# Performance work log

Hardware: AMD Instinct MI355X
Metric: run time of the kernel (lower is better)

Reference implementation:

```python
import jax, jax.numpy as jnp
import numpy as np

ENC_DIM = 1024
NUM_HEADS = 16
HEAD_DIM = ENC_DIM // NUM_HEADS
D_FF = 4 * ENC_DIM
EPS = 1e-5


def _layernorm(x, g, b):
    mu = jnp.mean(x, axis=-1, keepdims=True)
    var = jnp.mean((x - mu) ** 2, axis=-1, keepdims=True)
    return (x - mu) * jax.lax.rsqrt(var + EPS) * g + b


def setup_inputs() -> dict:
    key = jax.random.key(0)
    ks = jax.random.split(key, 12)
    s = 1.0 / np.sqrt(ENC_DIM)
    sf = 1.0 / np.sqrt(D_FF)
    x = jax.random.normal(ks[0], (2, 2048, ENC_DIM), dtype=jnp.float32)
    return {
        "x": x,
        "ln1_g": jnp.ones((ENC_DIM,), jnp.float32),
        "ln1_b": jnp.zeros((ENC_DIM,), jnp.float32),
        "wq": jax.random.uniform(ks[1], (ENC_DIM, ENC_DIM), jnp.float32, -s, s),
        "bq": jax.random.uniform(ks[2], (ENC_DIM,), jnp.float32, -s, s),
        "wk": jax.random.uniform(ks[3], (ENC_DIM, ENC_DIM), jnp.float32, -s, s),
        "bk": jax.random.uniform(ks[4], (ENC_DIM,), jnp.float32, -s, s),
        "wv": jax.random.uniform(ks[5], (ENC_DIM, ENC_DIM), jnp.float32, -s, s),
        "bv": jax.random.uniform(ks[6], (ENC_DIM,), jnp.float32, -s, s),
        "wo": jax.random.uniform(ks[7], (ENC_DIM, ENC_DIM), jnp.float32, -s, s),
        "bo": jax.random.uniform(ks[8], (ENC_DIM,), jnp.float32, -s, s),
        "w1": jax.random.uniform(ks[9], (ENC_DIM, D_FF), jnp.float32, -s, s),
        "b1": jax.random.uniform(ks[10], (D_FF,), jnp.float32, -s, s),
        "w2": jax.random.uniform(ks[11], (D_FF, ENC_DIM), jnp.float32, -sf, sf),
        "b2": jnp.zeros((ENC_DIM,), jnp.float32),
        "ln2_g": jnp.ones((ENC_DIM,), jnp.float32),
        "ln2_b": jnp.zeros((ENC_DIM,), jnp.float32),
    }


def reference(x, ln1_g, ln1_b, wq, bq, wk, bk, wv, bv, wo, bo, w1, b1, w2, b2, ln2_g, ln2_b):
    B, S, D = x.shape
    h = _layernorm(x, ln1_g, ln1_b)
    # QKV projections -> (B, H, S, hd)
    def split_heads(t):
        return t.reshape(B, S, NUM_HEADS, HEAD_DIM).transpose(0, 2, 1, 3)
    q = split_heads(h @ wq + bq)
    k = split_heads(h @ wk + bk)
    v = split_heads(h @ wv + bv)
    scores = jnp.einsum("bhqd,bhkd->bhqk", q, k) / np.sqrt(HEAD_DIM)
    probs = jax.nn.softmax(scores, axis=-1)
    attn = jnp.einsum("bhqk,bhkd->bhqd", probs, v)
    attn = attn.transpose(0, 2, 1, 3).reshape(B, S, D)
    x = attn @ wo + bo + x  # residual 1
    h2 = _layernorm(x, ln2_g, ln2_b)
    mlp = jax.nn.gelu(h2 @ w1 + b1, approximate=False) @ w2 + b2
    return x + mlp
```

## Files before the change

### kernel.cpp

```cpp
#include <hip/hip_runtime.h>

typedef unsigned short u16;
typedef unsigned int u32;
typedef __bf16 bf16x8 __attribute__((ext_vector_type(8)));
typedef float floatx4 __attribute__((ext_vector_type(4)));

__device__ __forceinline__ u16 f2bf(float f) {
    u32 u = __float_as_uint(f);
    u = (u + 0x7FFFu + ((u >> 16) & 1u)) >> 16;
    return (u16)u;
}

__device__ __forceinline__ void gld_lds16(const u16* g, u16* l) {
    __builtin_amdgcn_global_load_lds(
        (const __attribute__((address_space(1))) u32*)g,
        (__attribute__((address_space(3))) u32*)l, 16, 0, 0);
}

__device__ __forceinline__ float gelu_exact(float v) {
    const float z = fabsf(v) * 0.70710678118f;
    const float t = __builtin_amdgcn_rcpf(1.0f + 0.3275911f * z);
    const float e = __builtin_amdgcn_exp2f(-z * z * 1.44269504f);
    float poly = 1.061405429f;
    poly = poly * t - 1.453152027f;
    poly = poly * t + 1.421413741f;
    poly = poly * t - 0.284496736f;
    poly = poly * t + 0.254829592f;
    float erfz = 1.0f - poly * t * e;
    erfz = copysignf(erfz, v);
    return 0.5f * v * (1.0f + erfz);
}

__global__ __launch_bounds__(256) void transpose_cvt4(
    const float* __restrict__ s0, const float* __restrict__ s1,
    const float* __restrict__ s2, const float* __restrict__ s3,
    u16* __restrict__ d0, u16* __restrict__ d1,
    u16* __restrict__ d2, u16* __restrict__ d3)
{
    __shared__ float t[32][33];
    const int z = blockIdx.z;
    const float* src = z == 0 ? s0 : (z == 1 ? s1 : (z == 2 ? s2 : s3));
    u16* dst = z == 0 ? d0 : (z == 1 ? d1 : (z == 2 ? d2 : d3));
    const int bm = blockIdx.x * 32, bk = blockIdx.y * 32;
    const int tx = threadIdx.x & 31, ty = threadIdx.x >> 5;
    #pragma unroll
    for (int i = ty; i < 32; i += 8)
        t[i][tx] = src[(long)(bk + i) * 1024 + bm + tx];
    __syncthreads();
    #pragma unroll
    for (int i = ty; i < 32; i += 8)
        dst[(long)(bm + i) * 1024 + bk + tx] = f2bf(t[tx][i]);
}

__global__ __launch_bounds__(256) void transpose_cvt(
    const float* __restrict__ src, u16* __restrict__ dst, int K, int M)
{
    __shared__ float t[32][33];
    const int bm = blockIdx.x * 32, bk = blockIdx.y * 32;
    const int tx = threadIdx.x & 31, ty = threadIdx.x >> 5;
    #pragma unroll
    for (int i = ty; i < 32; i += 8)
        t[i][tx] = src[(long)(bk + i) * M + bm + tx];
    __syncthreads();
    #pragma unroll
    for (int i = ty; i < 32; i += 8)
        dst[(long)(bm + i) * K + bk + tx] = f2bf(t[tx][i]);
}

__global__ __launch_bounds__(256) void ln_kernel(
    const float* __restrict__ x, const float* __restrict__ g,
    const float* __restrict__ bta, u16* __restrict__ out)
{
    const int row = blockIdx.x;
    const int tid = threadIdx.x;
    const float4 v = ((const float4*)(x + (long)row * 1024))[tid];
    float s  = v.x + v.y + v.z + v.w;
    float s2 = v.x*v.x + v.y*v.y + v.z*v.z + v.w*v.w;
    #pragma unroll
    for (int off = 1; off < 64; off <<= 1) {
        s  += __shfl_xor(s, off);
        s2 += __shfl_xor(s2, off);
    }
    __shared__ float red[8];
    const int wave = tid >> 6, lane = tid & 63;
    if (lane == 0) { red[wave] = s; red[4 + wave] = s2; }
    __syncthreads();
    s  = red[0] + red[1] + red[2] + red[3];
    s2 = red[4] + red[5] + red[6] + red[7];
    const float mu   = s * (1.0f / 1024.0f);
    const float var  = s2 * (1.0f / 1024.0f) - mu * mu;
    const float rstd = rsqrtf(var + 1e-5f);
    const int c = tid << 2;
    ushort4 o;
    o.x = f2bf((v.x - mu) * rstd * g[c + 0] + bta[c + 0]);
    o.y = f2bf((v.y - mu) * rstd * g[c + 1] + bta[c + 1]);
    o.z = f2bf((v.z - mu) * rstd * g[c + 2] + bta[c + 2]);
    o.w = f2bf((v.w - mu) * rstd * g[c + 3] + bta[c + 3]);
    ((ushort4*)(out + (long)row * 1024))[tid] = o;
}

__global__ __launch_bounds__(256) void vtrans_kernel(
    const u16* __restrict__ V, u16* __restrict__ Vt)
{
    __shared__ u16 t[64][72];
    const int bh = blockIdx.y, s0 = blockIdx.x << 6;
    const int tid = threadIdx.x;
    const long base = (long)bh * 2048 * 64;
    const int row = tid >> 2, seg = tid & 3;
    *(uint4*)&t[row][seg << 3] =
        *(const uint4*)(V + base + (long)(s0 + row) * 64 + (seg << 3));
    *(uint4*)&t[row][(seg + 4) << 3] =
        *(const uint4*)(V + base + (long)(s0 + row) * 64 + ((seg + 4) << 3));
    __syncthreads();
    #pragma unroll
    for (int half = 0; half < 2; ++half) {
        const int sl = (seg + (half << 2)) << 3;
        u16 tmp[8];
        #pragma unroll
        for (int j = 0; j < 8; ++j) tmp[j] = t[sl + j][row];
        *(uint4*)(Vt + base + (long)row * 2048 + s0 + sl) = *(uint4*)tmp;
    }
}

template<int MODE>
__global__ __launch_bounds__(512, 2) void gemm256_kernel(
    const u16* __restrict__ A, const u16* __restrict__ Bt,
    const float* __restrict__ bias0, const float* __restrict__ bias1,
    const float* __restrict__ bias2, const float* __restrict__ res,
    float* __restrict__ outf, void* __restrict__ outv, int K, int M)
{
    __shared__ u16 As[2][256 * 64];
    __shared__ u16 Bs[2][256 * 64];
    const int tid = threadIdx.x, lane = tid & 63, wave = tid >> 6;
    const int wr = wave >> 2, wc = wave & 3;
    const int lrow = lane & 15, quad = lane >> 4, sl = lrow & 7;

    const int nwg = gridDim.x * gridDim.y * gridDim.z;
    const int lin = blockIdx.x + gridDim.x * (blockIdx.y + gridDim.y * blockIdx.z);
    const int wg  = (lin & 7) * (nwg >> 3) + (lin >> 3);
    const int bx  = wg % gridDim.x;
    const int rest = wg / gridDim.x;
    const int by  = rest % gridDim.y;
    const int bz  = rest / gridDim.y;

    const long rowbase = (long)by * 256;
    const long colbase = (long)bx * 256;
    int kstart = 0, kend = K;
    if constexpr (MODE == 3) { kstart = bz * (K >> 2); kend = kstart + (K >> 2); }

    const u16* gA[4]; int lA[4];
    const u16* gB[4]; int lB[4];
    #pragma unroll
    for (int i = 0; i < 4; ++i) {
        const int cid = (i << 9) + tid;
        const int rl = cid >> 3, p = cid & 7, q = p ^ (rl & 7);
        gA[i] = A  + (rowbase + rl) * (long)K + kstart + (q << 3);
        gB[i] = Bt + (colbase + rl) * (long)K + kstart + (q << 3);
        lA[i] = rl * 64 + (p << 3);
        lB[i] = rl * 64 + (p << 3);
    }

    floatx4 acc[8][4];
    #pragma unroll
    for (int i = 0; i < 8; ++i)
        #pragma unroll
        for (int j = 0; j < 4; ++j)
            acc[i][j] = floatx4{0.f, 0.f, 0.f, 0.f};

    #pragma unroll
    for (int i = 0; i < 4; ++i) { gld_lds16(gA[i], As[0] + lA[i]); gA[i] += 64; }
    #pragma unroll
    for (int i = 0; i < 4; ++i) { gld_lds16(gB[i], Bs[0] + lB[i]); gB[i] += 64; }
    asm volatile("s_waitcnt vmcnt(0)" ::: "memory");
    __builtin_amdgcn_s_barrier();
    __builtin_amdgcn_sched_barrier(0);

    const int niter = (kend - kstart) >> 6;
    int cur = 0;
    for (int t = 0; t < niter; ++t) {
        if (t + 1 < niter) {
            #pragma unroll
            for (int i = 0; i < 4; ++i) { gld_lds16(gA[i], As[cur ^ 1] + lA[i]); gA[i] += 64; }
            #pragma unroll
            for (int i = 0; i < 4; ++i) { gld_lds16(gB[i], Bs[cur ^ 1] + lB[i]); gB[i] += 64; }
        }

        const u16* as = As[cur];
        const u16* bs = Bs[cur];

        bf16x8 bfr[4][2];
        #pragma unroll
        for (int ns = 0; ns < 4; ++ns)
            #pragma unroll
            for (int kc = 0; kc < 2; ++kc)
                bfr[ns][kc] = *(const bf16x8*)
                    &bs[((wc << 6) + (ns << 4) + lrow) * 64 + ((((kc << 2) + quad) ^ sl) << 3)];

        #pragma unroll
        for (int p = 0; p < 4; ++p) {
            bf16x8 af[2][2];
            #pragma unroll
            for (int m = 0; m < 2; ++m)
                #pragma unroll
                for (int kc = 0; kc < 2; ++kc)
                    af[m][kc] = *(const bf16x8*)
                        &as[((wr << 7) + ((p * 2 + m) << 4) + lrow) * 64 + ((((kc << 2) + quad) ^ sl) << 3)];
            __builtin_amdgcn_s_setprio(1);
            #pragma unroll
            for (int kc = 0; kc < 2; ++kc)
                #pragma unroll
                for (int m = 0; m < 2; ++m)
                    #pragma unroll
                    for (int ns = 0; ns < 4; ++ns)
                        acc[p * 2 + m][ns] = __builtin_amdgcn_mfma_f32_16x16x32_bf16(
                            af[m][kc], bfr[ns][kc], acc[p * 2 + m][ns], 0, 0, 0);
            __builtin_amdgcn_s_setprio(0);
        }

        asm volatile("s_waitcnt lgkmcnt(0)" ::: "memory");
        asm volatile("s_waitcnt vmcnt(0)" ::: "memory");
        __builtin_amdgcn_s_barrier();
        __builtin_amdgcn_sched_barrier(0);
        cur ^= 1;
    }

    #pragma unroll
    for (int ms = 0; ms < 8; ++ms) {
        #pragma unroll
        for (int ns = 0; ns < 4; ++ns) {
            const long col = colbase + (wc << 6) + (ns << 4) + lrow;
            float bv = 0.f;
            if constexpr (MODE == 0) {
                const int which = (int)(col >> 10);
                const float* bp = which == 0 ? bias0 : (which == 1 ? bias1 : bias2);
                bv = bp[col & 1023];
            } else if constexpr (MODE == 2) {
                bv = bias0[col];
            }
            #pragma unroll
            for (int r = 0; r < 4; ++r) {
                const long row = rowbase + (wr << 7) + (ms << 4) + (quad << 2) + r;
                float v = acc[ms][ns][r] + bv;
                if constexpr (MODE == 0) {
                    const long which = col >> 10;
                    if (which == 0) v *= 0.18033688f;
                    const long b = row >> 11, s = row & 2047;
                    const long h = (col >> 6) & 15, d = col & 63;
                    ((u16*)outv)[which * 4194304 + (((b << 4) + h) * 2048 + s) * 64 + d] = f2bf(v);
                } else if constexpr (MODE == 2) {
                    ((u16*)outv)[row * M + col] = f2bf(gelu_exact(v));
                } else {
                    const long idx = row * M + col;
                    if (bz == 0) v += bias0[col] + res[idx];
                    atomicAdd(&outf[idx], v);
                }
            }
        }
    }
}

__global__ __launch_bounds__(256) void gemm_oproj_kernel(
    const u16* __restrict__ A, const u16* __restrict__ Bt,
    const float* __restrict__ bias0, const float* __restrict__ res,
    float* __restrict__ out, int K, int M)
{
    constexpr int MS = 2, NIB = 2;
    __shared__ u16 As[128 * 64];
    __shared__ u16 Bs[64 * 64];
    const int tid = threadIdx.x, lane = tid & 63, wave = tid >> 6;
    const int wm = wave << 5, wn = 0;
    const int lrow = lane & 15, quad = lane >> 4;
    const int sl = lrow & 7;

    const int nwg = gridDim.x * gridDim.y;
    const int lin = blockIdx.x + gridDim.x * blockIdx.y;
    const int wg  = (lin & 7) * (nwg >> 3) + (lin >> 3);
    const int bx  = wg % gridDim.x;
    const int by  = wg / gridDim.x;

    const long rowbase = (long)by * 128;
    const long colbase = (long)bx * 64;

    const u16* gA[4]; int lA[4];
    #pragma unroll
    for (int i = 0; i < 4; ++i) {
        const int cid = (i << 6) + lane;
        const int rl = cid >> 3, p = cid & 7, q = p ^ (rl & 7);
        gA[i] = A + (rowbase + (wave << 5) + rl) * (long)K + (q << 3);
        lA[i] = ((wave << 5) + rl) * 64 + (p << 3);
    }
    const u16* gB[NIB]; int lB[NIB];
    #pragma unroll
    for (int i = 0; i < NIB; ++i) {
        const int cid = (i << 6) + lane;
        const int rl = cid >> 3, p = cid & 7, q = p ^ (rl & 7);
        gB[i] = Bt + (colbase + (wave << 4) + rl) * (long)K + (q << 3);
        lB[i] = ((wave << 4) + rl) * 64 + (p << 3);
    }

    floatx4 acc[MS][4];
    #pragma unroll
    for (int i = 0; i < MS; ++i)
        #pragma unroll
        for (int j = 0; j < 4; ++j)
            acc[i][j] = floatx4{0.f, 0.f, 0.f, 0.f};

    for (int k0 = 0; k0 < K; k0 += 64) {
        __syncthreads();
        #pragma unroll
        for (int i = 0; i < 4; ++i) { gld_lds16(gA[i], As + lA[i]); gA[i] += 64; }
        #pragma unroll
        for (int i = 0; i < NIB; ++i) { gld_lds16(gB[i], Bs + lB[i]); gB[i] += 64; }
        __syncthreads();
        #pragma unroll
        for (int kc = 0; kc < 2; ++kc) {
            const int ph = (((kc << 2) + quad) ^ sl) << 3;
            bf16x8 af[MS], bf[4];
            #pragma unroll
            for (int ms = 0; ms < MS; ++ms)
                af[ms] = *(const bf16x8*)&As[(wm + (ms << 4) + lrow) * 64 + ph];
            #pragma unroll
            for (int ns = 0; ns < 4; ++ns)
                bf[ns] = *(const bf16x8*)&Bs[(wn + (ns << 4) + lrow) * 64 + ph];
            #pragma unroll
            for (int ms = 0; ms < MS; ++ms)
                #pragma unroll
                for (int ns = 0; ns < 4; ++ns)
                    acc[ms][ns] = __builtin_amdgcn_mfma_f32_16x16x32_bf16(
                        af[ms], bf[ns], acc[ms][ns], 0, 0, 0);
        }
    }

    #pragma unroll
    for (int ms = 0; ms < MS; ++ms) {
        #pragma unroll
        for (int ns = 0; ns < 4; ++ns) {
            const long col = colbase + wn + (ns << 4) + lrow;
            const float bv = bias0[col];
            #pragma unroll
            for (int r = 0; r < 4; ++r) {
                const long row = rowbase + wm + (ms << 4) + (quad << 2) + r;
                const long idx = row * M + col;
                out[idx] = acc[ms][ns][r] + bv + res[idx];
            }
        }
    }
}

__global__ __launch_bounds__(512) void attn_kernel(
    const u16* __restrict__ Q, const u16* __restrict__ Kp,
    const u16* __restrict__ Vt, u16* __restrict__ O)
{
    __shared__ u16 Ks[2][4096];
    __shared__ u16 Vs[2][4096];
    __shared__ u16 Ps[8][16][72];
    const int tid = threadIdx.x, lane = tid & 63, wave = tid >> 6;
    const int lrow = lane & 15, quad = lane >> 4;

    const int lin = blockIdx.x;
    const int nl  = ((lin & 7) << 6) + (lin >> 3);
    const int bh  = nl >> 4;
    const int qt  = nl & 15;
    const long kvbase = (long)bh * 2048 * 64;
    const int qbase = (qt << 7) + (wave << 4);

    const int srow = lane >> 3;
    const int schunk = (lane & 7) ^ srow;
    const int c = wave & 3;
    const bool isV = wave >= 4;
    const int lofs = c << 10;
    const u16* g0 = isV
        ? (Vt + kvbase + (long)(((c << 4) + srow) * 2048 + (schunk << 3)))
        : (Kp + kvbase + (long)(((c << 4) + srow) * 64   + (schunk << 3)));
    const u16* g1 = g0 + (isV ? 8 * 2048 : 8 * 64);
    const int gstep = isV ? 64 : 4096;
    u16* lb0 = isV ? &Vs[0][lofs] : &Ks[0][lofs];
    u16* lb1 = isV ? &Vs[1][lofs] : &Ks[1][lofs];

    bf16x8 qf[2];
    #pragma unroll
    for (int h = 0; h < 2; ++h)
        qf[h] = *(const bf16x8*)(Q + kvbase +
            (long)(qbase + lrow) * 64 + (quad << 3) + (h << 5));

    int aoff[4][2];
    #pragma unroll
    for (int ns = 0; ns < 4; ++ns)
        #pragma unroll
        for (int h = 0; h < 2; ++h)
            aoff[ns][h] = ((ns << 4) + lrow) * 64 +
                          (((quad + (h << 2)) ^ (lrow & 7)) << 3);

    floatx4 oacc[4];
    #pragma unroll
    for (int ns = 0; ns < 4; ++ns)
        oacc[ns] = floatx4{0.f, 0.f, 0.f, 0.f};
    float lr = 0.f;

    gld_lds16(g0, lb0);
    gld_lds16(g1, lb0 + 512);
    g0 += gstep; g1 += gstep;

    for (int it = 0; it < 32; ++it) {
        const int cur = it & 1;
        __syncthreads();
        if (it < 31) {
            u16* dst = cur ? lb0 : lb1;
            gld_lds16(g0, dst);
            gld_lds16(g1, dst + 512);
            g0 += gstep; g1 += gstep;
        }
        const u16* ks = &Ks[cur][0];
        const u16* vs = &Vs[cur][0];

        floatx4 st[4];
        __builtin_amdgcn_s_setprio(1);
        #pragma unroll
        for (int ns = 0; ns < 4; ++ns) {
            const bf16x8 af0 = *(const bf16x8*)&ks[aoff[ns][0]];
            const bf16x8 af1 = *(const bf16x8*)&ks[aoff[ns][1]];
            floatx4 z = floatx4{0.f, 0.f, 0.f, 0.f};
            st[ns] = __builtin_amdgcn_mfma_f32_16x16x32_bf16(af0, qf[0], z, 0, 0, 0);
            st[ns] = __builtin_amdgcn_mfma_f32_16x16x32_bf16(af1, qf[1], st[ns], 0, 0, 0);
        }
        __builtin_amdgcn_s_setprio(0);

        float rs = 0.f;
        #pragma unroll
        for (int ns = 0; ns < 4; ++ns) {
            const float p0 = __builtin_amdgcn_exp2f(st[ns][0]);
            const float p1 = __builtin_amdgcn_exp2f(st[ns][1]);
            const float p2 = __builtin_amdgcn_exp2f(st[ns][2]);
            const float p3 = __builtin_amdgcn_exp2f(st[ns][3]);
            rs += (p0 + p1) + (p2 + p3);
            uint2 w;
            w.x = __builtin_amdgcn_perm(__float_as_uint(p1) + 0x8000u,
                                        __float_as_uint(p0) + 0x8000u, 0x07060302u);
            w.y = __builtin_amdgcn_perm(__float_as_uint(p3) + 0x8000u,
                                        __float_as_uint(p2) + 0x8000u, 0x07060302u);
            *(uint2*)&Ps[wave][lrow][(ns << 4) + (quad << 2)] = w;
        }
        rs += __shfl_xor(rs, 16);
        rs += __shfl_xor(rs, 32);
        lr += rs;
        const bf16x8 pf0 = *(const bf16x8*)&Ps[wave][lrow][quad << 3];
        const bf16x8 pf1 = *(const bf16x8*)&Ps[wave][lrow][(quad << 3) + 32];

        __builtin_amdgcn_s_setprio(1);
        #pragma unroll
        for (int ns = 0; ns < 4; ++ns) {
            const bf16x8 vf0 = *(const bf16x8*)&vs[aoff[ns][0]];
            const bf16x8 vf1 = *(const bf16x8*)&vs[aoff[ns][1]];
            oacc[ns] = __builtin_amdgcn_mfma_f32_16x16x32_bf16(pf0, vf0, oacc[ns], 0, 0, 0);
            oacc[ns] = __builtin_amdgcn_mfma_f32_16x16x32_bf16(pf1, vf1, oacc[ns], 0, 0, 0);
        }
        __builtin_amdgcn_s_setprio(0);
    }

    const int b = bh >> 4, h = bh & 15;
    float linv[4];
    #pragma unroll
    for (int r = 0; r < 4; ++r)
        linv[r] = 1.0f / __shfl(lr, (quad << 2) + r);
    #pragma unroll
    for (int ns = 0; ns < 4; ++ns)
        #pragma unroll
        for (int r = 0; r < 4; ++r) {
            const int q = qbase + (quad << 2) + r;
            const long token = (long)b * 2048 + q;
            O[token * 1024 + (h << 6) + (ns << 4) + lrow] =
                f2bf(oacc[ns][r] * linv[r]);
        }
}

extern "C" void kernel_launch(void* const* d_in, const int* in_sizes, int n_in,
                              void* d_out, int out_size, void* d_ws, size_t ws_size,
                              hipStream_t stream)
{
    const float* x     = (const float*)d_in[0];
    const float* ln1_g = (const float*)d_in[1];
    const float* ln1_b = (const float*)d_in[2];
    const float* wq    = (const float*)d_in[3];
    const float* bq    = (const float*)d_in[4];
    const float* wk    = (const float*)d_in[5];
    const float* bk    = (const float*)d_in[6];
    const float* wv    = (const float*)d_in[7];
    const float* bv    = (const float*)d_in[8];
    const float* wo    = (const float*)d_in[9];
    const float* bo    = (const float*)d_in[10];
    const float* w1    = (const float*)d_in[11];
    const float* b1    = (const float*)d_in[12];
    const float* w2    = (const float*)d_in[13];
    const float* b2    = (const float*)d_in[14];
    const float* ln2_g = (const float*)d_in[15];
    const float* ln2_b = (const float*)d_in[16];
    float* out = (float*)d_out;

    char* w = (char*)d_ws;
    const size_t MB = 1024 * 1024;
    u16*   wqkvt = (u16*)(w + 0);
    u16*   wot   = (u16*)(w + 6  * MB);
    u16*   w1t   = (u16*)(w + 8  * MB);
    u16*   w2t   = (u16*)(w + 16 * MB);
    u16*   h1    = (u16*)(w + 24 * MB);
    u16*   qkvb  = (u16*)(w + 32 * MB);
    u16*   vtb   = (u16*)(w + 56 * MB);
    float* x1    = (float*)(w + 64 * MB);
    u16*   ffb   = (u16*)(w + 32 * MB);
    u16*   qb = qkvb;
    u16*   kb = qkvb + 4194304;
    u16*   vb = qkvb + 8388608;

    transpose_cvt4<<<dim3(32, 32, 4), 256, 0, stream>>>(
        wq, wk, wv, wo, wqkvt, wqkvt + 1048576, wqkvt + 2097152, wot);
    transpose_cvt<<<dim3(128, 32), 256, 0, stream>>>(w1, w1t, 1024, 4096);
    transpose_cvt<<<dim3(32, 128), 256, 0, stream>>>(w2, w2t, 4096, 1024);

    ln_kernel<<<4096, 256, 0, stream>>>(x, ln1_g, ln1_b, h1);

    gemm256_kernel<0><<<dim3(12, 16), 512, 0, stream>>>(
        h1, wqkvt, bq, bk, bv, nullptr, nullptr, qkvb, 1024, 3072);

    vtrans_kernel<<<dim3(32, 32), 256, 0, stream>>>(vb, vtb);

    attn_kernel<<<dim3(512), 512, 0, stream>>>(qb, kb, vtb, h1);

    gemm_oproj_kernel<<<dim3(16, 32), 256, 0, stream>>>(
        h1, wot, bo, x, x1, 1024, 1024);

    ln_kernel<<<4096, 256, 0, stream>>>(x1, ln2_g, ln2_b, h1);

    gemm256_kernel<2><<<dim3(16, 16), 512, 0, stream>>>(
        h1, w1t, b1, nullptr, nullptr, nullptr, nullptr, ffb, 1024, 4096);

    hipMemsetAsync(out, 0, (size_t)4096 * 1024 * 4, stream);
    gemm256_kernel<3><<<dim3(4, 16, 4), 512, 0, stream>>>(
        ffb, w2t, b2, nullptr, nullptr, x1, out, nullptr, 4096, 1024);
}
```

Measured before the change: 407.4 us.

## Replace atomic split-K FF2 GEMM with 128-tile 2-way split and add pass

The second MLP GEMM previously used 256x256 tiles with 4-way split-K, a memset of the output and atomicAdd epilogues. It now uses a dedicated 128x128-tile kernel with 2-way split-K. One half writes bias plus residual plus partial sum to the output and the other half writes to a scratch buffer, and a separate elementwise kernel then adds the two. This removes the memset and the atomic traffic, and the smaller tiles give 512 workgroups. In exchange there is an extra kernel launch, an extra full-tensor read/write pass, and less data reuse per tile.

Result: faster. 345.5 us (-15.2%).

```diff
diff --git a/kernel.cpp b/kernel.cpp
--- a/kernel.cpp
+++ b/kernel.cpp
@@ -99,6 +99,20 @@
     ((ushort4*)(out + (long)row * 1024))[tid] = o;
 }
 
+__global__ __launch_bounds__(256) void add_kernel(
+    float* __restrict__ out, const float* __restrict__ p1)
+{
+    const int t = blockIdx.x * 256 + threadIdx.x;
+    const float4 a = ((const float4*)out)[t];
+    const float4 c = ((const float4*)p1)[t];
+    float4 o;
+    o.x = a.x + c.x;
+    o.y = a.y + c.y;
+    o.z = a.z + c.z;
+    o.w = a.w + c.w;
+    ((float4*)out)[t] = o;
+}
+
 __global__ __launch_bounds__(256) void vtrans_kernel(
     const u16* __restrict__ V, u16* __restrict__ Vt)
 {
@@ -126,8 +140,7 @@
 __global__ __launch_bounds__(512, 2) void gemm256_kernel(
     const u16* __restrict__ A, const u16* __restrict__ Bt,
     const float* __restrict__ bias0, const float* __restrict__ bias1,
-    const float* __restrict__ bias2, const float* __restrict__ res,
-    float* __restrict__ outf, void* __restrict__ outv, int K, int M)
+    const float* __restrict__ bias2, void* __restrict__ outv, int K, int M)
 {
     __shared__ u16 As[2][256 * 64];
     __shared__ u16 Bs[2][256 * 64];
@@ -135,18 +148,14 @@
     const int wr = wave >> 2, wc = wave & 3;
     const int lrow = lane & 15, quad = lane >> 4, sl = lrow & 7;
 
-    const int nwg = gridDim.x * gridDim.y * gridDim.z;
-    const int lin = blockIdx.x + gridDim.x * (blockIdx.y + gridDim.y * blockIdx.z);
+    const int nwg = gridDim.x * gridDim.y;
+    const int lin = blockIdx.x + gridDim.x * blockIdx.y;
     const int wg  = (lin & 7) * (nwg >> 3) + (lin >> 3);
     const int bx  = wg % gridDim.x;
-    const int rest = wg / gridDim.x;
-    const int by  = rest % gridDim.y;
-    const int bz  = rest / gridDim.y;
+    const int by  = wg / gridDim.x;
 
     const long rowbase = (long)by * 256;
     const long colbase = (long)bx * 256;
-    int kstart = 0, kend = K;
-    if constexpr (MODE == 3) { kstart = bz * (K >> 2); kend = kstart + (K >> 2); }
 
     const u16* gA[4]; int lA[4];
     const u16* gB[4]; int lB[4];
@@ -154,8 +163,8 @@
     for (int i = 0; i < 4; ++i) {
         const int cid = (i << 9) + tid;
         const int rl = cid >> 3, p = cid & 7, q = p ^ (rl & 7);
-        gA[i] = A  + (rowbase + rl) * (long)K + kstart + (q << 3);
-        gB[i] = Bt + (colbase + rl) * (long)K + kstart + (q << 3);
+        gA[i] = A  + (rowbase + rl) * (long)K + (q << 3);
+        gB[i] = Bt + (colbase + rl) * (long)K + (q << 3);
         lA[i] = rl * 64 + (p << 3);
         lB[i] = rl * 64 + (p << 3);
     }
@@ -175,7 +184,7 @@
     __builtin_amdgcn_s_barrier();
     __builtin_amdgcn_sched_barrier(0);
 
-    const int niter = (kend - kstart) >> 6;
+    const int niter = K >> 6;
     int cur = 0;
     for (int t = 0; t < niter; ++t) {
         if (t + 1 < niter) {
@@ -229,12 +238,12 @@
         #pragma unroll
         for (int ns = 0; ns < 4; ++ns) {
             const long col = colbase + (wc << 6) + (ns << 4) + lrow;
-            float bv = 0.f;
+            float bv;
             if constexpr (MODE == 0) {
                 const int which = (int)(col >> 10);
                 const float* bp = which == 0 ? bias0 : (which == 1 ? bias1 : bias2);
                 bv = bp[col & 1023];
-            } else if constexpr (MODE == 2) {
+            } else {
                 bv = bias0[col];
             }
             #pragma unroll
@@ -247,13 +256,125 @@
                     const long b = row >> 11, s = row & 2047;
                     const long h = (col >> 6) & 15, d = col & 63;
                     ((u16*)outv)[which * 4194304 + (((b << 4) + h) * 2048 + s) * 64 + d] = f2bf(v);
-                } else if constexpr (MODE == 2) {
+                } else {
                     ((u16*)outv)[row * M + col] = f2bf(gelu_exact(v));
-                } else {
-                    const long idx = row * M + col;
-                    if (bz == 0) v += bias0[col] + res[idx];
-                    atomicAdd(&outf[idx], v);
                 }
+            }
+        }
+    }
+}
+
+__global__ __launch_bounds__(512, 2) void gemm_ff2_kernel(
+    const u16* __restrict__ A, const u16* __restrict__ Bt,
+    const float* __restrict__ bias0, const float* __restrict__ res,
+    float* __restrict__ part1, float* __restrict__ out, int K, int M)
+{
+    __shared__ u16 As[2][128 * 64];
+    __shared__ u16 Bs[2][128 * 64];
+    const int tid = threadIdx.x, lane = tid & 63, wave = tid >> 6;
+    const int wr = wave >> 2, wc = wave & 3;
+    const int lrow = lane & 15, quad = lane >> 4, sl = lrow & 7;
+
+    const int nwg = gridDim.x * gridDim.y * gridDim.z;
+    const int lin = blockIdx.x + gridDim.x * (blockIdx.y + gridDim.y * blockIdx.z);
+    const int wg  = (lin & 7) * (nwg >> 3) + (lin >> 3);
+    const int bx  = wg % gridDim.x;
+    const int rest = wg / gridDim.x;
+    const int by  = rest % gridDim.y;
+    const int bz  = rest / gridDim.y;
+
+    const long rowbase = (long)by * 128;
+    const long colbase = (long)bx * 128;
+    const int kstart = bz * (K >> 1);
+    const int kend   = kstart + (K >> 1);
+
+    const u16* gA[2]; int lA[2];
+    const u16* gB[2]; int lB[2];
+    #pragma unroll
+    for (int i = 0; i < 2; ++i) {
+        const int cid = (i << 9) + tid;
+        const int rl = cid >> 3, p = cid & 7, q = p ^ (rl & 7);
+        gA[i] = A  + (rowbase + rl) * (long)K + kstart + (q << 3);
+        gB[i] = Bt + (colbase + rl) * (long)K + kstart + (q << 3);
+        lA[i] = rl * 64 + (p << 3);
+        lB[i] = rl * 64 + (p << 3);
+    }
+
+    floatx4 acc[4][2];
+    #pragma unroll
+    for (int i = 0; i < 4; ++i)
+        #pragma unroll
+        for (int j = 0; j < 2; ++j)
+            acc[i][j] = floatx4{0.f, 0.f, 0.f, 0.f};
+
+    #pragma unroll
+    for (int i = 0; i < 2; ++i) { gld_lds16(gA[i], As[0] + lA[i]); gA[i] += 64; }
+    #pragma unroll
+    for (int i = 0; i < 2; ++i) { gld_lds16(gB[i], Bs[0] + lB[i]); gB[i] += 64; }
+    asm volatile("s_waitcnt vmcnt(0)" ::: "memory");
+    __builtin_amdgcn_s_barrier();
+    __builtin_amdgcn_sched_barrier(0);
+
+    const int niter = (kend - kstart) >> 6;
+    int cur = 0;
+    for (int t = 0; t < niter; ++t) {
+        if (t + 1 < niter) {
+            #pragma unroll
+            for (int i = 0; i < 2; ++i) { gld_lds16(gA[i], As[cur ^ 1] + lA[i]); gA[i] += 64; }
+            #pragma unroll
+            for (int i = 0; i < 2; ++i) { gld_lds16(gB[i], Bs[cur ^ 1] + lB[i]); gB[i] += 64; }
+        }
+
+        const u16* as = As[cur];
+        const u16* bs = Bs[cur];
+
+        bf16x8 bfr[2][2], af[4][2];
+        #pragma unroll
+        for (int ns = 0; ns < 2; ++ns)
+            #pragma unroll
+            for (int kc = 0; kc < 2; ++kc)
+                bfr[ns][kc] = *(const bf16x8*)
+                    &bs[((wc << 5) + (ns << 4) + lrow) * 64 + ((((kc << 2) + quad) ^ sl) << 3)];
+        #pragma unroll
+        for (int m = 0; m < 4; ++m)
+            #pragma unroll
+            for (int kc = 0; kc < 2; ++kc)
+                af[m][kc] = *(const bf16x8*)
+                    &as[((wr << 6) + (m << 4) + lrow) * 64 + ((((kc << 2) + quad) ^ sl) << 3)];
+
+        __builtin_amdgcn_s_setprio(1);
+        #pragma unroll
+        for (int kc = 0; kc < 2; ++kc)
+            #pragma unroll
+            for (int m = 0; m < 4; ++m)
+                #pragma unroll
+                for (int ns = 0; ns < 2; ++ns)
+                    acc[m][ns] = __builtin_amdgcn_mfma_f32_16x16x32_bf16(
+                        af[m][kc], bfr[ns][kc], acc[m][ns], 0, 0, 0);
+        __builtin_amdgcn_s_setprio(0);
+
+        asm volatile("s_waitcnt lgkmcnt(0)" ::: "memory");
+        asm volatile("s_waitcnt vmcnt(0)" ::: "memory");
+        __builtin_amdgcn_s_barrier();
+        __builtin_amdgcn_sched_barrier(0);
+        cur ^= 1;
+    }
+
+    float* tgt = bz ? part1 : out;
+    #pragma unroll
+    for (int m = 0; m < 4; ++m) {
+        #pragma unroll
+        for (int ns = 0; ns < 2; ++ns) {
+            const long col = colbase + (wc << 5) + (ns << 4) + lrow;
+            #pragma unroll
+            for (int r = 0; r < 4; ++r) {
+                const long row = rowbase + (wr << 6) + (m << 4) + (quad << 2) + r;
+                const long idx = row * M + col;
+                float v = acc[m][ns][r];
+                if (bz == 0)
+                    tgt[idx] = v + bias0[col] + res[idx];
+                else
+                    tgt[idx] = v;
             }
         }
     }
@@ -506,6 +627,7 @@
     u16*   qkvb  = (u16*)(w + 32 * MB);
     u16*   vtb   = (u16*)(w + 56 * MB);
     float* x1    = (float*)(w + 64 * MB);
+    float* part1 = (float*)(w + 80 * MB);
     u16*   ffb   = (u16*)(w + 32 * MB);
     u16*   qb = qkvb;
     u16*   kb = qkvb + 4194304;
@@ -519,7 +641,7 @@
     ln_kernel<<<4096, 256, 0, stream>>>(x, ln1_g, ln1_b, h1);
 
     gemm256_kernel<0><<<dim3(12, 16), 512, 0, stream>>>(
-        h1, wqkvt, bq, bk, bv, nullptr, nullptr, qkvb, 1024, 3072);
+        h1, wqkvt, bq, bk, bv, qkvb, 1024, 3072);
 
     vtrans_kernel<<<dim3(32, 32), 256, 0, stream>>>(vb, vtb);
 
@@ -531,9 +653,10 @@
     ln_kernel<<<4096, 256, 0, stream>>>(x1, ln2_g, ln2_b, h1);
 
     gemm256_kernel<2><<<dim3(16, 16), 512, 0, stream>>>(
-        h1, w1t, b1, nullptr, nullptr, nullptr, nullptr, ffb, 1024, 4096);
-
-    hipMemsetAsync(out, 0, (size_t)4096 * 1024 * 4, stream);
-    gemm256_kernel<3><<<dim3(4, 16, 4), 512, 0, stream>>>(
-        ffb, w2t, b2, nullptr, nullptr, x1, out, nullptr, 4096, 1024);
-}
+        h1, w1t, b1, nullptr, nullptr, ffb, 1024, 4096);
+
+    gemm_ff2_kernel<<<dim3(8, 32, 2), 512, 0, stream>>>(
+        ffb, w2t, b2, x1, part1, out, 4096, 1024);
+
+    add_kernel<<<4096, 256, 0, stream>>>(out, part1);
+}
```
